# Performance work log

Measured on AMD Instinct MI355X. Metric: run time of the kernel, lower is better.

The kernel has to match this reference:

```python
import jax, jax.numpy as jnp
import numpy as np

# Loss config: losses = [Supervised(weight=1), TemporalConsistency(padding=0.05, weight=1)]
PADDING_FRAC = 0.05
W_SUPERVISED = 1.0
W_TEMPORAL = 1.0


def setup_inputs() -> dict:
    key = jax.random.key(0)
    k1, k2 = jax.random.split(key)
    B, T, C, H, W = 4, 24, 4, 240, 320
    frames = jax.random.uniform(k1, (B, T, C, H, W), dtype=jnp.float32)
    # sparsify GT alpha so the (gt_alpha > 0) mask is non-trivial (fast-moving object occupies part of the frame)
    alpha = frames[:, :, 3:]
    frames = frames.at[:, :, 3:].set(jnp.where(alpha > 0.5, alpha, 0.0))
    renders = jax.random.uniform(k2, (B, T, C, H, W), dtype=jnp.float32)
    return {"frames": frames, "renders": renders}


def _l1(a, b, w, dims):
    # masked mean-abs-error over image dims, then mean over time axis 1 -> [B]
    err = jnp.sum(jnp.abs(a - b) * w, axis=dims)
    wsum = jnp.sum(w, axis=dims)
    wsum = wsum + (wsum == 0)  # avoid div by zero, matches torch weights + (weights==0)
    return (err / wsum).mean(axis=1)


def _supervised(frames, renders):
    gt_rgb, rend_rgb = frames[:, :, :3], renders[:, :, :3]
    gt_a, rend_a = frames[:, :, -1:], renders[:, :, -1:]
    mask = (gt_a > 0).astype(frames.dtype)
    dims = (2, 3, 4)
    alpha_in = _l1(gt_a, rend_a, mask, dims)
    alpha_out = _l1(gt_a, rend_a, 1.0 - mask, dims)
    rgb = _l1(gt_rgb * gt_a, rend_rgb * rend_a, mask, dims)
    return (alpha_in + alpha_out + rgb) / 3


def _normalize(t, dims):
    mean = t.mean(axis=dims, keepdims=True)
    std = t.std(axis=dims, keepdims=True)  # ddof=0 == torch unbiased=False
    std = std + (std == 0)
    return (t - mean) / std


def _zncc(a, b, pad):
    # a, b: [B, T, C, H, W]; per-(b,t) zero-normalized cross-correlation over (dy, dx) shifts
    B, T, C, H, W = a.shape
    dims = (2, 3, 4)
    a = _normalize(a, dims)
    b = _normalize(b, dims)
    BT = B * T
    lhs = a.reshape(1, BT, C, H, W)     # N=1, channels=BT, spatial=(C,H,W)
    rhs = b.reshape(BT, 1, C, H, W)     # one full-size kernel per group
    cc = jax.lax.conv_general_dilated(
        lhs, rhs,
        window_strides=(1, 1, 1),
        padding=[(0, 0), (pad, pad), (pad, pad)],
        dimension_numbers=("NCDHW", "OIDHW", "NCDHW"),
        feature_group_count=BT,
    )  # [1, BT, 1, 2p+1, 2p+1]; jax conv is cross-correlation like torch
    cc = cc / (C * H * W)
    return cc.reshape(B, T, cc.shape[-2], cc.shape[-1])


def _temporal_consistency(renders):
    pad = int(PADDING_FRAC * renders.shape[-1])
    z = _zncc(renders[:, :-1], renders[:, 1:], pad)  # [B, T-1, 2p+1, 2p+1]
    return (1.0 - z.max(axis=(2, 3)).mean(axis=1)) / 2


def reference(frames, renders):
    sup = _supervised(frames, renders) * W_SUPERVISED
    tc = _temporal_consistency(renders) * W_TEMPORAL
    return jnp.stack([sup, tc], axis=1)  # [B, n_losses=2]
```

## Files before the change

### kernel.cpp

```cpp
#include <hip/hip_runtime.h>
#include <hip/hip_bf16.h>

#define B_    4
#define T_    24
#define C_    4
#define H_    240
#define W_    320
#define HW_   (H_*W_)
#define CHW_  (C_*HW_)
#define NF_   (B_*T_)
#define NPAIR_ (B_*(T_-1))
#define PAD_  16
#define ND_   33
#define HC_   16
#define NCH_  15

constexpr int PART_OFF = 0;
constexpr int MEAN_OFF = PART_OFF + NF_*8*6;
constexpr int ISTD_OFF = MEAN_OFF + NF_;
constexpr int Z_OFF    = ISTD_OFF + NF_;
constexpr int ZMAX_OFF = Z_OFF + NPAIR_*ND_*ND_;

typedef __attribute__((ext_vector_type(8))) __bf16 bf16x8;
typedef __attribute__((ext_vector_type(4))) float  f32x4;
typedef __attribute__((ext_vector_type(8))) unsigned short ushort8;

static __device__ __forceinline__ unsigned short f2bf(float f) {
  unsigned u = __builtin_bit_cast(unsigned, f);
  unsigned r = (u + 0x7FFFu + ((u >> 16) & 1u)) >> 16;
  return (unsigned short)r;
}
static __device__ __forceinline__ unsigned pk2(float lo, float hi) {
  return (unsigned)f2bf(lo) | ((unsigned)f2bf(hi) << 16);
}

__global__ __launch_bounds__(256) void sup_stats_kernel(
    const float* __restrict__ frames, const float* __restrict__ renders,
    float* __restrict__ ws) {
  const int f = blockIdx.x >> 3;
  const int s = blockIdx.x & 7;
  const float* Fb = frames  + (size_t)f * CHW_;
  const float* Rb = renders + (size_t)f * CHW_;
  const int p0 = s * (HW_ / 8);
  float S1 = 0.f, S2 = 0.f, S3 = 0.f, MS = 0.f, SR = 0.f, SQ = 0.f;
  for (int q = (int)threadIdx.x; q < (HW_ / 8) / 4; q += 256) {
    const int p = p0 + q * 4;
    float4 f0 = *(const float4*)(Fb + p);
    float4 f1 = *(const float4*)(Fb + HW_ + p);
    float4 f2 = *(const float4*)(Fb + 2 * HW_ + p);
    float4 fa = *(const float4*)(Fb + 3 * HW_ + p);
    float4 r0 = *(const float4*)(Rb + p);
    float4 r1 = *(const float4*)(Rb + HW_ + p);
    float4 r2 = *(const float4*)(Rb + 2 * HW_ + p);
    float4 ra = *(const float4*)(Rb + 3 * HW_ + p);
    const float F0[4] = {f0.x, f0.y, f0.z, f0.w};
    const float F1[4] = {f1.x, f1.y, f1.z, f1.w};
    const float F2[4] = {f2.x, f2.y, f2.z, f2.w};
    const float FA[4] = {fa.x, fa.y, fa.z, fa.w};
    const float R0[4] = {r0.x, r0.y, r0.z, r0.w};
    const float R1[4] = {r1.x, r1.y, r1.z, r1.w};
    const float R2[4] = {r2.x, r2.y, r2.z, r2.w};
    const float RA[4] = {ra.x, ra.y, ra.z, ra.w};
    #pragma unroll
    for (int k = 0; k < 4; ++k) {
      float m = (FA[k] > 0.f) ? 1.f : 0.f;
      float d = fabsf(FA[k] - RA[k]);
      S1 = fmaf(d, m, S1);
      S2 = fmaf(d, 1.f - m, S2);
      MS += m;
      float e = fabsf(F0[k] * FA[k] - R0[k] * RA[k]) +
                fabsf(F1[k] * FA[k] - R1[k] * RA[k]) +
                fabsf(F2[k] * FA[k] - R2[k] * RA[k]);
      S3 = fmaf(e, m, S3);
      SR += R0[k] + R1[k] + R2[k] + RA[k];
      SQ += R0[k] * R0[k] + R1[k] * R1[k] + R2[k] * R2[k] + RA[k] * RA[k];
    }
  }
  __shared__ float sm[4];
  float vals[6] = {S1, S2, S3, MS, SR, SQ};
  float* dst = ws + PART_OFF + (size_t)(f * 8 + s) * 6;
  const int wv = threadIdx.x >> 6, ln = threadIdx.x & 63;
  for (int k = 0; k < 6; ++k) {
    float v = vals[k];
    #pragma unroll
    for (int o = 32; o >= 1; o >>= 1) v += __shfl_down(v, o);
    __syncthreads();
    if (ln == 0) sm[wv] = v;
    __syncthreads();
    if (threadIdx.x == 0) dst[k] = sm[0] + sm[1] + sm[2] + sm[3];
  }
}

__global__ __launch_bounds__(128) void finalize_stats_kernel(
    float* __restrict__ ws, float* __restrict__ out) {
  __shared__ float term_s[NF_];
  const int f = threadIdx.x;
  if (f < NF_) {
    float S1 = 0, S2 = 0, S3 = 0, MS = 0, SR = 0, SQ = 0;
    for (int s = 0; s < 8; ++s) {
      const float* p = ws + PART_OFF + (size_t)(f * 8 + s) * 6;
      S1 += p[0]; S2 += p[1]; S3 += p[2]; MS += p[3]; SR += p[4]; SQ += p[5];
    }
    float mean = SR * (1.f / (float)CHW_);
    float var  = SQ * (1.f / (float)CHW_) - mean * mean;
    float sd   = sqrtf(fmaxf(var, 0.f));
    if (sd == 0.f) sd = 1.f;
    ws[MEAN_OFF + f] = mean;
    ws[ISTD_OFF + f] = 1.f / sd;
    float w1 = MS;               if (w1 == 0.f) w1 = 1.f;
    float w2 = (float)HW_ - MS;  if (w2 == 0.f) w2 = 1.f;
    term_s[f] = (S1 / w1 + S2 / w2 + S3 / w1) * (1.f / 3.f);
  }
  __syncthreads();
  if (threadIdx.x < B_) {
    float acc = 0.f;
    for (int t = 0; t < T_; ++t) acc += term_s[threadIdx.x * T_ + t];
    out[2 * threadIdx.x] = acc * (1.f / (float)T_);
  }
}

__global__ __launch_bounds__(512, 4) void zncc_mfma_kernel(
    const float* __restrict__ renders, float* __restrict__ ws) {
  const int pair  = blockIdx.x / NCH_;
  const int chunk = blockIdx.x - pair * NCH_;
  const int h0 = chunk * HC_;
  const int bb = pair / (T_ - 1);
  const int tt = pair - bb * (T_ - 1);
  const int fa = bb * T_ + tt;
  const int fb = fa + 1;
  const float ma = ws[MEAN_OFF + fa], ia = ws[ISTD_OFF + fa];
  const float mb = ws[MEAN_OFF + fb], ib = ws[ISTD_OFF + fb];
  const int tid = threadIdx.x;
  const int wv = tid >> 6, ln = tid & 63;
  const int g = ln >> 4, r = ln & 15;

  __shared__ alignas(16) unsigned short a_su[64 * 328];
  __shared__ alignas(16) unsigned bs_[HC_][368];

  f32x4 acc[3][3];
  #pragma unroll
  for (int mi = 0; mi < 3; ++mi)
    #pragma unroll
    for (int ni = 0; ni < 3; ++ni)
      acc[mi][ni] = (f32x4){0.f, 0.f, 0.f, 0.f};

  for (int c = 0; c < C_; ++c) {
    __syncthreads();
    {
      const float* Ag = renders + ((size_t)fa * C_ + c) * HW_;
      for (int q = tid; q < 64 * 40; q += 512) {
        const int si = q / 40;
        const int j8 = (q - si * 40) << 3;
        const int gr = h0 - 16 + si;
        ushort8 sv = (ushort8)0;
        if (gr >= 0 && gr < H_) {
          const float* src = Ag + (size_t)gr * W_ + j8;
          float4 v0 = *(const float4*)(src);
          float4 v1 = *(const float4*)(src + 4);
          sv[0] = f2bf((v0.x - ma) * ia); sv[1] = f2bf((v0.y - ma) * ia);
          sv[2] = f2bf((v0.z - ma) * ia); sv[3] = f2bf((v0.w - ma) * ia);
          sv[4] = f2bf((v1.x - ma) * ia); sv[5] = f2bf((v1.y - ma) * ia);
          sv[6] = f2bf((v1.z - ma) * ia); sv[7] = f2bf((v1.w - ma) * ia);
        }
        *(ushort8*)(a_su + si * 328 + j8) = sv;
      }
    }
    {
      const float* Bg = renders + ((size_t)fb * C_ + c) * HW_;
      for (int xq = tid; xq < HC_ * 92; xq += 512) {
        const int hr = xq / 92;
        const int x0 = (xq - hr * 92) << 2;
        const float* brow = Bg + (size_t)(h0 + hr) * W_;
        float wv5[5];
        const int wbase = x0 - 32;
        #pragma unroll
        for (int k = 0; k < 5; ++k) {
          const int ww = wbase + k;
          wv5[k] = (ww >= 0 && ww < W_) ? (brow[ww] - mb) * ib : 0.f;
        }
        uint4 pk;
        pk.x = pk2(wv5[0], wv5[1]);
        pk.y = pk2(wv5[1], wv5[2]);
        pk.z = pk2(wv5[2], wv5[3]);
        pk.w = pk2(wv5[3], wv5[4]);
        *(uint4*)&bs_[hr][x0] = pk;
      }
    }
    __syncthreads();
    for (int ho = 0; ho < 2; ++ho) {
      const int hh = ho * 8 + wv;
      const unsigned* bsrow = &bs_[hh][0];
      const unsigned short* arow = a_su + (hh + r) * 328 + g * 8;
      #pragma unroll
      for (int kw = 0; kw < 10; ++kw) {
        bf16x8 af[3];
        #pragma unroll
        for (int mi = 0; mi < 3; ++mi)
          af[mi] = *(const bf16x8*)(arow + mi * (16 * 328) + kw * 32);
        bf16x8 bfr[3];
        #pragma unroll
        for (int ni = 0; ni < 3; ++ni) {
          const int pe = 32 * kw + 8 * g + 48 - 16 * ni - r;
          union { unsigned u[4]; bf16x8 v; } bu;
          bu.u[0] = bsrow[pe];
          bu.u[1] = bsrow[pe + 2];
          bu.u[2] = bsrow[pe + 4];
          bu.u[3] = bsrow[pe + 6];
          bfr[ni] = bu.v;
        }
        #pragma unroll
        for (int mi = 0; mi < 3; ++mi)
          #pragma unroll
          for (int ni = 0; ni < 3; ++ni)
            acc[mi][ni] = __builtin_amdgcn_mfma_f32_16x16x32_bf16(
                af[mi], bfr[ni], acc[mi][ni], 0, 0, 0);
      }
    }
  }

  __syncthreads();
  f32x4* red = (f32x4*)a_su;
  if (wv >= 4) {
    f32x4* dst = red + ((wv - 4) * 64 + ln) * 9;
    #pragma unroll
    for (int mi = 0; mi < 3; ++mi)
      #pragma unroll
      for (int ni = 0; ni < 3; ++ni)
        dst[mi * 3 + ni] = acc[mi][ni];
  }
  __syncthreads();
  if (wv < 4) {
    const f32x4* src = red + (wv * 64 + ln) * 9;
    #pragma unroll
    for (int mi = 0; mi < 3; ++mi)
      #pragma unroll
      for (int ni = 0; ni < 3; ++ni)
        acc[mi][ni] += src[mi * 3 + ni];
    float* z = ws + Z_OFF + (size_t)pair * (ND_ * ND_);
    #pragma unroll
    for (int mi = 0; mi < 3; ++mi) {
      #pragma unroll
      for (int i = 0; i < 4; ++i) {
        const int m = 16 * mi + 4 * g + i;
        if (m < ND_) {
          #pragma unroll
          for (int ni = 0; ni < 3; ++ni) {
            const int n = 16 * ni + r;
            if (n < ND_)
              atomicAdd(&z[m * ND_ + n], acc[mi][ni][i] * (1.f / (float)CHW_));
          }
        }
      }
    }
  }
}

__global__ __launch_bounds__(256) void tc_max_kernel(
    const float* __restrict__ ws, float* __restrict__ wso) {
  const int pair = blockIdx.x;
  const float* z = ws + Z_OFF + (size_t)pair * (ND_ * ND_);
  float m = -3.4e38f;
  for (int i = threadIdx.x; i < ND_ * ND_; i += 256) m = fmaxf(m, z[i]);
  #pragma unroll
  for (int o = 32; o >= 1; o >>= 1) m = fmaxf(m, __shfl_down(m, o));
  __shared__ float sm[4];
  const int wv = threadIdx.x >> 6, ln = threadIdx.x & 63;
  if (ln == 0) sm[wv] = m;
  __syncthreads();
  if (threadIdx.x == 0)
    wso[ZMAX_OFF + pair] = fmaxf(fmaxf(sm[0], sm[1]), fmaxf(sm[2], sm[3]));
}

__global__ __launch_bounds__(128) void tc_final_kernel(
    const float* __restrict__ ws, float* __restrict__ out) {
  if (threadIdx.x < B_) {
    float s = 0.f;
    for (int t = 0; t < T_ - 1; ++t)
      s += ws[ZMAX_OFF + threadIdx.x * (T_ - 1) + t];
    out[2 * threadIdx.x + 1] = (1.f - s * (1.f / (float)(T_ - 1))) * 0.5f;
  }
}

extern "C" void kernel_launch(void* const* d_in, const int* in_sizes, int n_in,
                              void* d_out, int out_size, void* d_ws, size_t ws_size,
                              hipStream_t stream) {
  const float* frames  = (const float*)d_in[0];
  const float* renders = (const float*)d_in[1];
  float* out = (float*)d_out;
  float* ws  = (float*)d_ws;
  hipLaunchKernelGGL(sup_stats_kernel, dim3(NF_ * 8), dim3(256), 0, stream,
                     frames, renders, ws);
  hipLaunchKernelGGL(finalize_stats_kernel, dim3(1), dim3(128), 0, stream, ws, out);
  hipMemsetAsync((char*)d_ws + (size_t)Z_OFF * 4, 0,
                 (size_t)NPAIR_ * ND_ * ND_ * 4, stream);
  hipLaunchKernelGGL(zncc_mfma_kernel, dim3(NPAIR_ * NCH_), dim3(512), 0, stream,
                     renders, ws);
  hipLaunchKernelGGL(tc_max_kernel, dim3(NPAIR_), dim3(256), 0, stream, ws, ws);
  hipLaunchKernelGGL(tc_final_kernel, dim3(1), dim3(128), 0, stream, ws, out);
}
```

Measured before the change: 433.1 us.

## Fold z-buffer zeroing into stats kernel, merge tail kernels, share B fragments via shuffle

The z accumulator is now zeroed inside sup_stats_kernel instead of by a separate hipMemsetAsync, and the per-pair max and final-mean kernels are merged into one per-batch kernel. Together these remove two launches. In the MFMA inner loop, three B-fragment LDS gathers per kw are replaced by one gather. The other two fragments come from the previous iteration's registers and a cross-half-wave shuffle, which cuts LDS traffic but adds shuffle and select instructions and relies on the fragment-offset algebra being correct.

New measurement: 449.1 us. 1.04x slower.

```diff
diff --git a/kernel.cpp b/kernel.cpp
--- a/kernel.cpp
+++ b/kernel.cpp
@@ -19,7 +19,6 @@
 constexpr int MEAN_OFF = PART_OFF + NF_*8*6;
 constexpr int ISTD_OFF = MEAN_OFF + NF_;
 constexpr int Z_OFF    = ISTD_OFF + NF_;
-constexpr int ZMAX_OFF = Z_OFF + NPAIR_*ND_*ND_;
 
 typedef __attribute__((ext_vector_type(8))) __bf16 bf16x8;
 typedef __attribute__((ext_vector_type(4))) float  f32x4;
@@ -37,6 +36,10 @@
 __global__ __launch_bounds__(256) void sup_stats_kernel(
     const float* __restrict__ frames, const float* __restrict__ renders,
     float* __restrict__ ws) {
+  if (blockIdx.x < NPAIR_) {
+    float* z = ws + Z_OFF + (size_t)blockIdx.x * (ND_ * ND_);
+    for (int i = threadIdx.x; i < ND_ * ND_; i += 256) z[i] = 0.f;
+  }
   const int f = blockIdx.x >> 3;
   const int s = blockIdx.x & 7;
   const float* Fb = frames  + (size_t)f * CHW_;
@@ -171,18 +174,18 @@
         const int hr = xq / 92;
         const int x0 = (xq - hr * 92) << 2;
         const float* brow = Bg + (size_t)(h0 + hr) * W_;
-        float wv5[5];
+        float v[5];
         const int wbase = x0 - 32;
         #pragma unroll
         for (int k = 0; k < 5; ++k) {
           const int ww = wbase + k;
-          wv5[k] = (ww >= 0 && ww < W_) ? (brow[ww] - mb) * ib : 0.f;
+          v[k] = (ww >= 0 && ww < W_) ? (brow[ww] - mb) * ib : 0.f;
         }
         uint4 pk;
-        pk.x = pk2(wv5[0], wv5[1]);
-        pk.y = pk2(wv5[1], wv5[2]);
-        pk.z = pk2(wv5[2], wv5[3]);
-        pk.w = pk2(wv5[3], wv5[4]);
+        pk.x = pk2(v[0], v[1]);
+        pk.y = pk2(v[1], v[2]);
+        pk.z = pk2(v[2], v[3]);
+        pk.w = pk2(v[3], v[4]);
         *(uint4*)&bs_[hr][x0] = pk;
       }
     }
@@ -191,29 +194,39 @@
       const int hh = ho * 8 + wv;
       const unsigned* bsrow = &bs_[hh][0];
       const unsigned short* arow = a_su + (hh + r) * 328 + g * 8;
+      const unsigned* bpA = bsrow + (8 * g + 48 - r);
+      const unsigned* bpB = bpA + 256;
+      uint4 prev, cur;
+      {
+        const unsigned* p = bsrow + (8 * g + 16 - r);
+        prev.x = p[0]; prev.y = p[2]; prev.z = p[4]; prev.w = p[6];
+      }
       #pragma unroll
       for (int kw = 0; kw < 10; ++kw) {
-        bf16x8 af[3];
+        const unsigned* p = (kw < 8) ? bpA : bpB;
+        const int off = 32 * kw - (kw < 8 ? 0 : 256);
+        cur.x = p[off];     cur.y = p[off + 2];
+        cur.z = p[off + 4]; cur.w = p[off + 6];
+        uint4 mx, b1;
+        mx.x = (ln < 32) ? cur.x : prev.x;
+        mx.y = (ln < 32) ? cur.y : prev.y;
+        mx.z = (ln < 32) ? cur.z : prev.z;
+        mx.w = (ln < 32) ? cur.w : prev.w;
+        b1.x = (unsigned)__shfl_xor((int)mx.x, 32, 64);
+        b1.y = (unsigned)__shfl_xor((int)mx.y, 32, 64);
+        b1.z = (unsigned)__shfl_xor((int)mx.z, 32, 64);
+        b1.w = (unsigned)__shfl_xor((int)mx.w, 32, 64);
+        union { uint4 u; bf16x8 v; } f0u, f1u, f2u;
+        f0u.u = cur; f1u.u = b1; f2u.u = prev;
+        bf16x8 bfr0 = f0u.v, bfr1 = f1u.v, bfr2 = f2u.v;
         #pragma unroll
-        for (int mi = 0; mi < 3; ++mi)
-          af[mi] = *(const bf16x8*)(arow + mi * (16 * 328) + kw * 32);
-        bf16x8 bfr[3];
-        #pragma unroll
-        for (int ni = 0; ni < 3; ++ni) {
-          const int pe = 32 * kw + 8 * g + 48 - 16 * ni - r;
-          union { unsigned u[4]; bf16x8 v; } bu;
-          bu.u[0] = bsrow[pe];
-          bu.u[1] = bsrow[pe + 2];
-          bu.u[2] = bsrow[pe + 4];
-          bu.u[3] = bsrow[pe + 6];
-          bfr[ni] = bu.v;
+        for (int mi = 0; mi < 3; ++mi) {
+          bf16x8 af = *(const bf16x8*)(arow + mi * (16 * 328) + kw * 32);
+          acc[mi][0] = __builtin_amdgcn_mfma_f32_16x16x32_bf16(af, bfr0, acc[mi][0], 0, 0, 0);
+          acc[mi][1] = __builtin_amdgcn_mfma_f32_16x16x32_bf16(af, bfr1, acc[mi][1], 0, 0, 0);
+          acc[mi][2] = __builtin_amdgcn_mfma_f32_16x16x32_bf16(af, bfr2, acc[mi][2], 0, 0, 0);
         }
-        #pragma unroll
-        for (int mi = 0; mi < 3; ++mi)
-          #pragma unroll
-          for (int ni = 0; ni < 3; ++ni)
-            acc[mi][ni] = __builtin_amdgcn_mfma_f32_16x16x32_bf16(
-                af[mi], bfr[ni], acc[mi][ni], 0, 0, 0);
+        prev = cur;
       }
     }
   }
@@ -255,29 +268,27 @@
   }
 }
 
-__global__ __launch_bounds__(256) void tc_max_kernel(
-    const float* __restrict__ ws, float* __restrict__ wso) {
-  const int pair = blockIdx.x;
-  const float* z = ws + Z_OFF + (size_t)pair * (ND_ * ND_);
-  float m = -3.4e38f;
-  for (int i = threadIdx.x; i < ND_ * ND_; i += 256) m = fmaxf(m, z[i]);
-  #pragma unroll
-  for (int o = 32; o >= 1; o >>= 1) m = fmaxf(m, __shfl_down(m, o));
-  __shared__ float sm[4];
+__global__ __launch_bounds__(512) void tc_kernel(
+    const float* __restrict__ ws, float* __restrict__ out) {
+  const int b = blockIdx.x;
   const int wv = threadIdx.x >> 6, ln = threadIdx.x & 63;
-  if (ln == 0) sm[wv] = m;
+  __shared__ float psum[8];
+  float s = 0.f;
+  for (int t = wv; t < T_ - 1; t += 8) {
+    const float* z = ws + Z_OFF + (size_t)(b * (T_ - 1) + t) * (ND_ * ND_);
+    float m = -3.4e38f;
+    for (int i = ln; i < ND_ * ND_; i += 64) m = fmaxf(m, z[i]);
+    #pragma unroll
+    for (int o = 32; o >= 1; o >>= 1) m = fmaxf(m, __shfl_xor(m, o));
+    s += m;
+  }
+  if (ln == 0) psum[wv] = s;
   __syncthreads();
-  if (threadIdx.x == 0)
-    wso[ZMAX_OFF + pair] = fmaxf(fmaxf(sm[0], sm[1]), fmaxf(sm[2], sm[3]));
-}
-
-__global__ __launch_bounds__(128) void tc_final_kernel(
-    const float* __restrict__ ws, float* __restrict__ out) {
-  if (threadIdx.x < B_) {
-    float s = 0.f;
-    for (int t = 0; t < T_ - 1; ++t)
-      s += ws[ZMAX_OFF + threadIdx.x * (T_ - 1) + t];
-    out[2 * threadIdx.x + 1] = (1.f - s * (1.f / (float)(T_ - 1))) * 0.5f;
+  if (threadIdx.x == 0) {
+    float tot = 0.f;
+    #pragma unroll
+    for (int w = 0; w < 8; ++w) tot += psum[w];
+    out[2 * b + 1] = (1.f - tot * (1.f / (float)(T_ - 1))) * 0.5f;
   }
 }
 
@@ -291,10 +302,7 @@
   hipLaunchKernelGGL(sup_stats_kernel, dim3(NF_ * 8), dim3(256), 0, stream,
                      frames, renders, ws);
   hipLaunchKernelGGL(finalize_stats_kernel, dim3(1), dim3(128), 0, stream, ws, out);
-  hipMemsetAsync((char*)d_ws + (size_t)Z_OFF * 4, 0,
-                 (size_t)NPAIR_ * ND_ * ND_ * 4, stream);
   hipLaunchKernelGGL(zncc_mfma_kernel, dim3(NPAIR_ * NCH_), dim3(512), 0, stream,
                      renders, ws);
-  hipLaunchKernelGGL(tc_max_kernel, dim3(NPAIR_), dim3(256), 0, stream, ws, ws);
-  hipLaunchKernelGGL(tc_final_kernel, dim3(1), dim3(128), 0, stream, ws, out);
-}
+  hipLaunchKernelGGL(tc_kernel, dim3(B_), dim3(512), 0, stream, ws, out);
+}
```
